# Optimization experiments

Hardware: AMD Instinct MI355X
Metric: run time of the kernel (lower is better)

## Reference

```python
import jax, jax.numpy as jnp
import numpy as np

B, D, H, DM, O = 8192, 512, 1024, 2048, 256


def setup_inputs() -> dict:
    key = jax.random.key(0)
    ks = jax.random.split(key, 24)
    def rn(k, shape, scale=1.0):
        return jax.random.normal(k, shape, dtype=jnp.float32) * scale
    w = 0.02  # weight init scale
    return {
        "x":  rn(ks[0], (B, D)),
        "h0": rn(ks[1], (B, H), 0.1), "h1": rn(ks[2], (B, H), 0.1),
        "c0": rn(ks[3], (B, H), 0.1), "c1": rn(ks[4], (B, H), 0.1),
        # Bernoulli keep masks with model_prob=1.0 -> all ones
        "m0": jnp.ones((B, H), jnp.float32), "m1": jnp.ones((B, H), jnp.float32),
        # layer 0 gate weights: in = D + H = 1536
        "Wf0": rn(ks[5], (D + H, H), w), "bf0": jnp.full((H,), 0.01, jnp.float32),
        "Wi0": rn(ks[6], (D + H, H), w), "bi0": jnp.full((H,), 0.01, jnp.float32),
        "Wc0": rn(ks[7], (D + H, H), w), "bc0": jnp.full((H,), 0.01, jnp.float32),
        "Wo0": rn(ks[8], (D + H, H), w), "bo0": jnp.full((H,), 0.01, jnp.float32),
        # layer 1 gate weights: in = H + H = 2048
        "Wf1": rn(ks[9],  (2 * H, H), w), "bf1": jnp.full((H,), 0.01, jnp.float32),
        "Wi1": rn(ks[10], (2 * H, H), w), "bi1": jnp.full((H,), 0.01, jnp.float32),
        "Wc1": rn(ks[11], (2 * H, H), w), "bc1": jnp.full((H,), 0.01, jnp.float32),
        "Wo1": rn(ks[12], (2 * H, H), w), "bo1": jnp.full((H,), 0.01, jnp.float32),
        # output MLP: H -> DM -> O (identity activation per default nn.Sequential())
        "Wm1": rn(ks[13], (H, DM), w), "bm1": jnp.full((DM,), 0.01, jnp.float32),
        "Wm2": rn(ks[14], (DM, O), w), "bm2": jnp.full((O,), 0.01, jnp.float32),
    }


def _lstm_cell(comb, c, Wf, bf, Wi, bi, Wc, bc, Wo, bo):
    # fuse the 4 gate GEMMs into one matmul, then split
    W = jnp.concatenate([Wf, Wi, Wc, Wo], axis=1)      # [in, 4H]
    b = jnp.concatenate([bf, bi, bc, bo])               # [4H]
    g = comb @ W + b                                    # [B, 4H]
    f, i, ct, o = jnp.split(g, 4, axis=1)
    c_new = jax.nn.sigmoid(f) * c + jax.nn.sigmoid(i) * jnp.tanh(ct)
    h_new = jax.nn.sigmoid(o) * jnp.tanh(c_new)
    return h_new, c_new


def reference(x, h0, h1, c0, c1, m0, m1,
              Wf0, bf0, Wi0, bi0, Wc0, bc0, Wo0, bo0,
              Wf1, bf1, Wi1, bi1, Wc1, bc1, Wo1, bo1,
              Wm1, bm1, Wm2, bm2):
    # layer 0: combined = cat(input, h0 * mask0)
    comb0 = jnp.concatenate([x, h0 * m0], axis=1)       # [B, D+H]
    h0n, c0n = _lstm_cell(comb0, c0, Wf0, bf0, Wi0, bi0, Wc0, bc0, Wo0, bo0)
    # layer 1: combined = cat(h0_new * mask0, h1 * mask1)
    comb1 = jnp.concatenate([h0n * m0, h1 * m1], axis=1)  # [B, 2H]
    h1n, c1n = _lstm_cell(comb1, c1, Wf1, bf1, Wi1, bi1, Wc1, bc1, Wo1, bo1)
    # output MLP (dropout p=0 is identity; activation is identity Sequential)
    out = (h1n @ Wm1 + bm1) @ Wm2 + bm2                 # [B, O]
    return out, h0n, h1n, c0n, c1n
```

## Files before the change

kernel.cpp:

```cpp
#include <hip/hip_runtime.h>
#include <hip/hip_bf16.h>
#include <cstdint>
#include <cstddef>

#define DI __device__ __forceinline__

typedef __attribute__((ext_vector_type(8))) short short8;
typedef __attribute__((ext_vector_type(4))) float f32x4;

static constexpr int Bb = 8192, Dd = 512, Hh = 1024;

DI short f2b(float f) {
  union { __hip_bfloat16 h; short s; } u;
  u.h = __float2bfloat16(f);
  return u.s;
}

DI float sigm(float x) {
  float e = __builtin_amdgcn_exp2f(-1.4426950408889634f * x);
  return __builtin_amdgcn_rcpf(1.0f + e);
}
DI float tanh_(float x) {
  float xc = fminf(fmaxf(x, -20.0f), 20.0f);
  float e = __builtin_amdgcn_exp2f(-2.8853900817779268f * xc);
  return (1.0f - e) * __builtin_amdgcn_rcpf(1.0f + e);
}

DI void gload16(const void* g, void* l) {
  __builtin_amdgcn_global_load_lds(
      (const __attribute__((address_space(1))) uint32_t*)g,
      (__attribute__((address_space(3))) uint32_t*)l, 16, 0, 0);
}


__global__ void conv_acts(const float* __restrict__ x, const float* __restrict__ h0,
                          const float* __restrict__ m0, const float* __restrict__ h1,
                          const float* __restrict__ m1,
                          short* __restrict__ A0, short* __restrict__ A1) {
  const int row = blockIdx.x, t = threadIdx.x;
  float v[8];
  if (t < 192) {
    if (t < 64) {
      const float4* p = (const float4*)(x + (size_t)row * Dd + t * 8);
      float4 a = p[0], b = p[1];
      v[0] = a.x; v[1] = a.y; v[2] = a.z; v[3] = a.w;
      v[4] = b.x; v[5] = b.y; v[6] = b.z; v[7] = b.w;
    } else {
      const int j = t * 8 - 512;
      const float4* ph = (const float4*)(h0 + (size_t)row * Hh + j);
      const float4* pm = (const float4*)(m0 + (size_t)row * Hh + j);
      float4 a = ph[0], b = ph[1], ma = pm[0], mb = pm[1];
      v[0] = a.x * ma.x; v[1] = a.y * ma.y; v[2] = a.z * ma.z; v[3] = a.w * ma.w;
      v[4] = b.x * mb.x; v[5] = b.y * mb.y; v[6] = b.z * mb.z; v[7] = b.w * mb.w;
    }
    short8 o;
    #pragma unroll
    for (int q = 0; q < 8; q++) o[q] = f2b(v[q]);
    *(short8*)(A0 + (size_t)row * 1536 + t * 8) = o;
  } else {
    const int j = (t - 192) * 8;
    const float4* ph = (const float4*)(h1 + (size_t)row * Hh + j);
    const float4* pm = (const float4*)(m1 + (size_t)row * Hh + j);
    float4 a = ph[0], b = ph[1], ma = pm[0], mb = pm[1];
    v[0] = a.x * ma.x; v[1] = a.y * ma.y; v[2] = a.z * ma.z; v[3] = a.w * ma.w;
    v[4] = b.x * mb.x; v[5] = b.y * mb.y; v[6] = b.z * mb.z; v[7] = b.w * mb.w;
    short8 o;
    #pragma unroll
    for (int q = 0; q < 8; q++) o[q] = f2b(v[q]);
    *(short8*)(A1 + (size_t)row * 2048 + 1024 + j) = o;
  }
}

__global__ void transpose_conv4(const float* __restrict__ s0, const float* __restrict__ s1,
                                const float* __restrict__ s2, const float* __restrict__ s3,
                                short* __restrict__ dst, int N, int K) {
  __shared__ float t[64][65];
  const int g = blockIdx.z;
  const float* src = (g == 0) ? s0 : (g == 1) ? s1 : (g == 2) ? s2 : s3;
  const int k0 = blockIdx.x * 64, n0 = blockIdx.y * 64;
  const int tid = threadIdx.x;
  const int r = tid >> 2, c0 = (tid & 3) * 16;
  const float* s = src + (size_t)(k0 + r) * N + n0 + c0;
  #pragma unroll
  for (int q = 0; q < 16; q += 4) {
    float4 v = *(const float4*)(s + q);
    t[r][c0 + q + 0] = v.x; t[r][c0 + q + 1] = v.y;
    t[r][c0 + q + 2] = v.z; t[r][c0 + q + 3] = v.w;
  }
  __syncthreads();
  const int n = n0 + r;
  const int j = (n >> 4) * 64 + g * 16 + (n & 15);
  short8 o0, o1;
  #pragma unroll
  for (int q = 0; q < 8; q++) o0[q] = f2b(t[c0 + q][r]);
  #pragma unroll
  for (int q = 0; q < 8; q++) o1[q] = f2b(t[c0 + 8 + q][r]);
  short* d = dst + (size_t)j * K + k0 + c0;
  *(short8*)d = o0;
  *((short8*)d + 1) = o1;
}

__global__ void transpose_conv(const float* __restrict__ src, short* __restrict__ dst,
                               int N, int K) {
  __shared__ float t[64][65];
  const int k0 = blockIdx.x * 64, n0 = blockIdx.y * 64;
  const int tid = threadIdx.x;
  const int r = tid >> 2, c0 = (tid & 3) * 16;
  const float* s = src + (size_t)(k0 + r) * N + n0 + c0;
  #pragma unroll
  for (int q = 0; q < 16; q += 4) {
    float4 v = *(const float4*)(s + q);
    t[r][c0 + q + 0] = v.x; t[r][c0 + q + 1] = v.y;
    t[r][c0 + q + 2] = v.z; t[r][c0 + q + 3] = v.w;
  }
  __syncthreads();
  const int n = n0 + r;
  short8 o0, o1;
  #pragma unroll
  for (int q = 0; q < 8; q++) o0[q] = f2b(t[c0 + q][r]);
  #pragma unroll
  for (int q = 0; q < 8; q++) o1[q] = f2b(t[c0 + 8 + q][r]);
  short* d = dst + (size_t)n * K + k0 + c0;
  *(short8*)d = o0;
  *((short8*)d + 1) = o1;
}

__global__ void conv_plain(const float* __restrict__ src, short* __restrict__ dst, int n8) {
  const int id = blockIdx.x * blockDim.x + threadIdx.x;
  if (id >= n8) return;
  const float4* p = (const float4*)(src + (size_t)id * 8);
  float4 a = p[0], b = p[1];
  short8 o;
  o[0] = f2b(a.x); o[1] = f2b(a.y); o[2] = f2b(a.z); o[3] = f2b(a.w);
  o[4] = f2b(b.x); o[5] = f2b(b.y); o[6] = f2b(b.z); o[7] = f2b(b.w);
  *(short8*)(dst + (size_t)id * 8) = o;
}

__global__ void bp_init(const float* __restrict__ bm2, float* __restrict__ bp) {
  bp[threadIdx.x] = bm2[threadIdx.x];
}
__global__ void bp_acc(const float* __restrict__ bm1, const float* __restrict__ Wm2,
                       float* __restrict__ bp) {
  const int o = threadIdx.x;
  const int k0 = blockIdx.x * 64;
  float s = 0.f;
  #pragma unroll 4
  for (int k = 0; k < 64; k++) s += bm1[k0 + k] * Wm2[(size_t)(k0 + k) * 256 + o];
  atomicAdd(&bp[o], s);
}

__global__ __launch_bounds__(256) void gemm_bt0(
    const short* __restrict__ A, const short* __restrict__ Bt, int K,
    short* __restrict__ Cb, int ldc) {
  __shared__ __align__(16) short sA[128 * 32];
  __shared__ __align__(16) short sB[128 * 32];
  const int tid = threadIdx.x;
  const int lane = tid & 63;
  const int wave = tid >> 6;
  const int wm = wave >> 1, wn = wave & 1;
  const int bm = blockIdx.x, bn = blockIdx.y;
  const int lr = lane & 15, lq = lane >> 4;

  f32x4 acc[4][4] = {};

  const short* pA = A + ((size_t)(bm * 128 + (tid >> 2))) * K + (tid & 3) * 8;
  const short* pB = Bt + ((size_t)(bn * 128 + (tid >> 2))) * K + (tid & 3) * 8;
  short* lA = sA + tid * 8;
  short* lB = sB + tid * 8;
  const int aoff = (wm * 64 + lr) * 32 + lq * 8;
  const int boff = (wn * 64 + lr) * 32 + lq * 8;

  for (int k0 = 0; k0 < K; k0 += 32) {
    gload16(pA + k0, lA);
    gload16(pA + (size_t)64 * K + k0, lA + 2048);
    gload16(pB + k0, lB);
    gload16(pB + (size_t)64 * K + k0, lB + 2048);
    __syncthreads();
    short8 af[4], bv[4];
    #pragma unroll
    for (int m = 0; m < 4; m++) af[m] = *(const short8*)&sA[aoff + m * 512];
    #pragma unroll
    for (int n = 0; n < 4; n++) bv[n] = *(const short8*)&sB[boff + n * 512];
    #pragma unroll
    for (int m = 0; m < 4; m++)
      #pragma unroll
      for (int n = 0; n < 4; n++)
        acc[m][n] = __builtin_amdgcn_mfma_f32_16x16x32_bf16(af[m], bv[n], acc[m][n], 0, 0, 0);
    __syncthreads();
  }

  const int crow0 = bm * 128 + wm * 64 + lq * 4;
  const int ccol0 = bn * 128 + wn * 64 + lr;
  #pragma unroll
  for (int m = 0; m < 4; m++)
    #pragma unroll
    for (int r = 0; r < 4; r++) {
      const int row = crow0 + m * 16 + r;
      #pragma unroll
      for (int n = 0; n < 4; n++)
        Cb[(size_t)row * ldc + ccol0 + n * 16] = f2b(acc[m][n][r]);
    }
}

__global__ __launch_bounds__(256) void gemm_out(
    const short* __restrict__ A, const short* __restrict__ Bt, int K,
    float* __restrict__ outp, const float* __restrict__ bpv) {
  __shared__ __align__(16) short sA[64 * 32];
  __shared__ __align__(16) short sB[128 * 32];
  const int tid = threadIdx.x;
  const int lane = tid & 63;
  const int wn = tid >> 6;
  const int bm = blockIdx.x, bn = blockIdx.y;
  const int lr = lane & 15, lq = lane >> 4;

  f32x4 acc[4][2] = {};

  const short* pA = A + ((size_t)(bm * 64 + (tid >> 2))) * K + (tid & 3) * 8;
  const short* pB = Bt + ((size_t)(bn * 128 + (tid >> 2))) * K + (tid & 3) * 8;
  short* lA = sA + tid * 8;
  short* lB = sB + tid * 8;
  const int boff = (wn * 32 + lr) * 32 + lq * 8;

  for (int k0 = 0; k0 < K; k0 += 32) {
    gload16(pA + k0, lA);
    gload16(pB + k0, lB);
    gload16(pB + (size_t)64 * K + k0, lB + 2048);
    __syncthreads();
    short8 af[4], bv[2];
    #pragma unroll
    for (int m = 0; m < 4; m++) af[m] = *(const short8*)&sA[(m * 16 + lr) * 32 + lq * 8];
    #pragma unroll
    for (int n = 0; n < 2; n++) bv[n] = *(const short8*)&sB[boff + n * 512];
    #pragma unroll
    for (int m = 0; m < 4; m++)
      #pragma unroll
      for (int n = 0; n < 2; n++)
        acc[m][n] = __builtin_amdgcn_mfma_f32_16x16x32_bf16(af[m], bv[n], acc[m][n], 0, 0, 0);
    __syncthreads();
  }

  const int crow0 = bm * 64 + lq * 4;
  const int ccol0 = bn * 128 + wn * 32 + lr;
  float bvv[2];
  #pragma unroll
  for (int n = 0; n < 2; n++) bvv[n] = bpv[ccol0 + n * 16];
  #pragma unroll
  for (int m = 0; m < 4; m++)
    #pragma unroll
    for (int r = 0; r < 4; r++) {
      const int row = crow0 + m * 16 + r;
      #pragma unroll
      for (int n = 0; n < 2; n++)
        outp[(size_t)row * 256 + ccol0 + n * 16] = acc[m][n][r] + bvv[n];
    }
}


#define STA(buf, h, kt) { const short* s_ = gA + (size_t)(h) * 64 * K + (size_t)(kt) * 64; \
    gload16(s_ + aS0, &sA[buf][h][tid * 8]);                                               \
    gload16(s_ + aS1, &sA[buf][h][4096 + tid * 8]); }
#define STB(buf, h, kt) { const short* s_ = gB + (size_t)(h) * 128 * K + (size_t)(kt) * 64; \
    gload16(s_ + bS0, &sB[buf][h][tid * 8]);                                                \
    gload16(s_ + bS1, &sB[buf][h][4096 + tid * 8]); }

#define LDB(buf) {                                                \
    const short* bb = &sB[buf][bh][brb];                          \
    _Pragma("unroll") for (int n = 0; n < 4; n++) {               \
      bv[n][0] = *(const short8*)(bb + n * 1024 + sw0);           \
      bv[n][1] = *(const short8*)(bb + n * 1024 + sw1); } }

#define LDA_(buf, q, av) {                                        \
    const short* ab = &sA[buf][(q) >> 1][arb + ((q) & 1) * 2048]; \
    av[0][0] = *(const short8*)(ab + sw0);                        \
    av[0][1] = *(const short8*)(ab + sw1);                        \
    av[1][0] = *(const short8*)(ab + 1024 + sw0);                 \
    av[1][1] = *(const short8*)(ab + 1024 + sw1); }

#define MM(q, av) {                                               \
    __builtin_amdgcn_s_setprio(1);                                \
    _Pragma("unroll") for (int m = 0; m < 2; m++)                 \
    _Pragma("unroll") for (int n = 0; n < 4; n++) {               \
      acc[2*(q)+m][n] = __builtin_amdgcn_mfma_f32_16x16x32_bf16(av[m][0], bv[n][0], acc[2*(q)+m][n], 0, 0, 0); \
      acc[2*(q)+m][n] = __builtin_amdgcn_mfma_f32_16x16x32_bf16(av[m][1], bv[n][1], acc[2*(q)+m][n], 0, 0, 0); } \
    __builtin_amdgcn_s_setprio(0); }

#define BARR() __builtin_amdgcn_s_barrier()
#define VM6()  asm volatile("s_waitcnt vmcnt(6)")
#define LG0()  asm volatile("s_waitcnt lgkmcnt(0)")

__global__ __launch_bounds__(512, 2) void gemm8_lstm(
    const short* __restrict__ A, const short* __restrict__ Bt, const int K,
    const float* __restrict__ cprev, float* __restrict__ hout,
    float* __restrict__ cout, short* __restrict__ anext, const int ldan,
    const float* __restrict__ mask,
    const float* __restrict__ bF, const float* __restrict__ bI,
    const float* __restrict__ bC, const float* __restrict__ bO) {
  __shared__ __align__(16) short sA[2][2][8192];
  __shared__ __align__(16) short sB[2][2][8192];
  const int tid = threadIdx.x;
  const int lane = tid & 63, wid = tid >> 6;
  const int wr = wid >> 2, wc = wid & 3;
  const int lr = lane & 15, lq = lane >> 4;
  const int bm = blockIdx.x, bn = blockIdx.y;

  const int NT = K >> 6;
  const int NIT = NT >> 1;

  const int r0 = tid >> 3;
  const int csw = (tid & 7) ^ (r0 & 7);
  const int growA0 = ((r0 >> 5) & 1) * 32 + (r0 & 31);
  const int growA1 = 128 + growA0;
  const size_t aS0 = (size_t)growA0 * K + csw * 8;
  const size_t aS1 = (size_t)growA1 * K + csw * 8;
  const size_t bS0 = (size_t)r0 * K + csw * 8;
  const size_t bS1 = (size_t)(r0 + 64) * K + csw * 8;
  const short* gA = A + (size_t)bm * 256 * K;
  const short* gB = Bt + (size_t)bn * 256 * K;

  const int arb = (wr * 64 + lr) * 64;
  const int brb = ((wc & 1) * 64 + lr) * 64;
  const int bh = wc >> 1;
  const int sw0 = ((lq) ^ (lr & 7)) * 8;
  const int sw1 = ((4 + lq) ^ (lr & 7)) * 8;

  f32x4 acc[8][4] = {};
  short8 bv[4][2];

  STB(0, 0, 0); STB(0, 1, 0); STA(0, 0, 0); STA(0, 1, 0);
  STB(1, 0, 1); STB(1, 1, 1); STA(1, 0, 1);
  VM6(); BARR();

  for (int it = 0; it < NIT; ++it) {
    const int k1 = 2 * it + 1;
    int t2 = 2 * it + 2; if (t2 >= NT) t2 = 0;
    int t3 = 2 * it + 3; if (t3 >= NT) t3 = 1;
    { short8 av0[2][2], av1[2][2];
      LDB(0); LDA_(0, 0, av0); LDA_(0, 1, av1); STA(1, 1, k1);
      BARR(); LG0(); MM(0, av0); MM(1, av1); BARR(); }
    { short8 av0[2][2], av1[2][2];
      LDA_(0, 2, av0); LDA_(0, 3, av1);
      STB(0, 0, t2); STB(0, 1, t2); STA(0, 0, t2);
      VM6(); BARR(); LG0(); MM(2, av0); MM(3, av1); BARR(); }
    { short8 av0[2][2], av1[2][2];
      LDB(1); LDA_(1, 0, av0); LDA_(1, 1, av1); STA(0, 1, t2);
      BARR(); LG0(); MM(0, av0); MM(1, av1); BARR(); }
    { short8 av0[2][2], av1[2][2];
      LDA_(1, 2, av0); LDA_(1, 3, av1);
      STB(1, 0, t3); STB(1, 1, t3); STA(1, 0, t3);
      VM6(); BARR(); LG0(); MM(2, av0); MM(3, av1); BARR(); }
  }

  const int n = (bn * 4 + wc) * 16 + lr;
  const float bf_ = bF[n], bi_ = bI[n], bc_ = bC[n], bo_ = bO[n];
  const int row0 = bm * 256 + wr * 128 + lq * 4;

  float cp[4], mk[4], cpn[4], mkn[4];
  #pragma unroll
  for (int rr = 0; rr < 4; rr++) {
    const size_t idx = (size_t)(row0 + rr) * 1024 + n;
    cp[rr] = cprev[idx];
    mk[rr] = mask ? mask[idx] : 1.0f;
  }
  #pragma unroll
  for (int mf = 0; mf < 8; mf++) {
    if (mf < 7) {
      #pragma unroll
      for (int rr = 0; rr < 4; rr++) {
        const size_t idx2 = (size_t)(row0 + (mf + 1) * 16 + rr) * 1024 + n;
        cpn[rr] = cprev[idx2];
        mkn[rr] = mask ? mask[idx2] : 1.0f;
      }
    }
    #pragma unroll
    for (int rr = 0; rr < 4; rr++) {
      const int row = row0 + mf * 16 + rr;
      const size_t idx = (size_t)row * 1024 + n;
      const float fg = sigm(acc[mf][0][rr] + bf_);
      const float ig = sigm(acc[mf][1][rr] + bi_);
      const float cg = tanh_(acc[mf][2][rr] + bc_);
      const float og = sigm(acc[mf][3][rr] + bo_);
      const float cn = fg * cp[rr] + ig * cg;
      const float hn = og * tanh_(cn);
      cout[idx] = cn;
      hout[idx] = hn;
      anext[(size_t)row * ldan + n] = f2b(hn * mk[rr]);
    }
    #pragma unroll
    for (int rr = 0; rr < 4; rr++) { cp[rr] = cpn[rr]; mk[rr] = mkn[rr]; }
  }
}


extern "C" void kernel_launch(void* const* d_in, const int* in_sizes, int n_in,
                              void* d_out, int out_size, void* d_ws, size_t ws_size,
                              hipStream_t stream) {
  (void)in_sizes; (void)n_in; (void)out_size; (void)ws_size;
  const float* x   = (const float*)d_in[0];
  const float* h0  = (const float*)d_in[1];
  const float* h1  = (const float*)d_in[2];
  const float* c0  = (const float*)d_in[3];
  const float* c1  = (const float*)d_in[4];
  const float* m0  = (const float*)d_in[5];
  const float* m1  = (const float*)d_in[6];
  const float* Wf0 = (const float*)d_in[7];  const float* bf0 = (const float*)d_in[8];
  const float* Wi0 = (const float*)d_in[9];  const float* bi0 = (const float*)d_in[10];
  const float* Wc0 = (const float*)d_in[11]; const float* bc0 = (const float*)d_in[12];
  const float* Wo0 = (const float*)d_in[13]; const float* bo0 = (const float*)d_in[14];
  const float* Wf1 = (const float*)d_in[15]; const float* bf1 = (const float*)d_in[16];
  const float* Wi1 = (const float*)d_in[17]; const float* bi1 = (const float*)d_in[18];
  const float* Wc1 = (const float*)d_in[19]; const float* bc1 = (const float*)d_in[20];
  const float* Wo1 = (const float*)d_in[21]; const float* bo1 = (const float*)d_in[22];
  const float* Wm1 = (const float*)d_in[23]; const float* bm1 = (const float*)d_in[24];
  const float* Wm2 = (const float*)d_in[25]; const float* bm2 = (const float*)d_in[26];

  float* dout  = (float*)d_out;
  float* out_o = dout;
  float* h0n   = dout + 2097152;
  float* h1n   = h0n + 8388608;
  float* c0n   = h1n + 8388608;
  float* c1n   = c0n + 8388608;

  char* ws = (char*)d_ws;
  short* A0   = (short*)(ws);
  short* A1   = (short*)(ws + 25165824);
  short* A2   = (short*)(ws + 58720256);
  short* WT0  = (short*)(ws + 75497472);
  short* WT1  = (short*)(ws + 88080384);
  short* Wm1b = (short*)(ws + 104857600);
  short* Wm2T = (short*)(ws + 109051904);
  short* WpT  = (short*)(ws + 110100480);
  float* bp   = (float*)(ws + 110624768);

  conv_acts<<<dim3(8192), dim3(320), 0, stream>>>(x, h0, m0, h1, m1, A0, A1);
  transpose_conv4<<<dim3(24, 16, 4), dim3(256), 0, stream>>>(Wf0, Wi0, Wc0, Wo0, WT0, 1024, 1536);
  transpose_conv4<<<dim3(32, 16, 4), dim3(256), 0, stream>>>(Wf1, Wi1, Wc1, Wo1, WT1, 1024, 2048);
  conv_plain<<<dim3(1024), dim3(256), 0, stream>>>(Wm1, Wm1b, 262144);
  transpose_conv<<<dim3(32, 4), dim3(256), 0, stream>>>(Wm2, Wm2T, 256, 2048);
  bp_init<<<dim3(1), dim3(256), 0, stream>>>(bm2, bp);
  bp_acc<<<dim3(32), dim3(256), 0, stream>>>(bm1, Wm2, bp);

  gemm_bt0<<<dim3(2, 8), dim3(256), 0, stream>>>(Wm2T, Wm1b, 2048, WpT, 1024);

  gemm8_lstm<<<dim3(32, 16), dim3(512), 0, stream>>>(
      A0, WT0, 1536, c0, h0n, c0n, A1, 2048, m0, bf0, bi0, bc0, bo0);

  gemm8_lstm<<<dim3(32, 16), dim3(512), 0, stream>>>(
      A1, WT1, 2048, c1, h1n, c1n, A2, 1024, nullptr, bf1, bi1, bc1, bo1);

  gemm_out<<<dim3(128, 2), dim3(256), 0, stream>>>(A2, WpT, 1024, out_o, bp);
}
```

Baseline: 406.6 us.

## Merge weight-prep kernels and spread global-to-LDS stores across finer MFMA phases

Six preprocessing launches (two gate-weight transposes, Wm1 conversion, Wm2 transpose, bias init and accumulate) become two kernels: one transposes both layers' gate weights and one handles all MLP prep, including a non-atomic bias reduction. This cuts launch overhead and idle tails between small kernels. The LSTM GEMM main loop now runs eight phases per iteration instead of four, each with one A fragment load and one staged global store, plus a partial lgkmcnt wait. The aim is to interleave memory traffic more evenly with MFMA work, at the price of twice as many barriers per iteration.

```diff
diff --git a/kernel.cpp b/kernel.cpp
--- a/kernel.cpp
+++ b/kernel.cpp
@@ -71,16 +71,30 @@
   }
 }
 
-__global__ void transpose_conv4(const float* __restrict__ s0, const float* __restrict__ s1,
-                                const float* __restrict__ s2, const float* __restrict__ s3,
-                                short* __restrict__ dst, int N, int K) {
+__global__ void transpose_all(
+    const float* __restrict__ w00, const float* __restrict__ w01,
+    const float* __restrict__ w02, const float* __restrict__ w03,
+    const float* __restrict__ w10, const float* __restrict__ w11,
+    const float* __restrict__ w12, const float* __restrict__ w13,
+    short* __restrict__ WT0, short* __restrict__ WT1) {
   __shared__ float t[64][65];
-  const int g = blockIdx.z;
-  const float* src = (g == 0) ? s0 : (g == 1) ? s1 : (g == 2) ? s2 : s3;
-  const int k0 = blockIdx.x * 64, n0 = blockIdx.y * 64;
+  const int z = blockIdx.z;
+  const int layer = z >> 2, g = z & 3;
+  const int K = layer ? 2048 : 1536;
+  const int k0 = blockIdx.x * 64;
+  if (k0 >= K) return;
+  const float* src;
+  switch (z) {
+    case 0: src = w00; break; case 1: src = w01; break;
+    case 2: src = w02; break; case 3: src = w03; break;
+    case 4: src = w10; break; case 5: src = w11; break;
+    case 6: src = w12; break; default: src = w13; break;
+  }
+  short* dst = layer ? WT1 : WT0;
+  const int n0 = blockIdx.y * 64;
   const int tid = threadIdx.x;
   const int r = tid >> 2, c0 = (tid & 3) * 16;
-  const float* s = src + (size_t)(k0 + r) * N + n0 + c0;
+  const float* s = src + (size_t)(k0 + r) * 1024 + n0 + c0;
   #pragma unroll
   for (int q = 0; q < 16; q += 4) {
     float4 v = *(const float4*)(s + q);
@@ -100,53 +114,59 @@
   *((short8*)d + 1) = o1;
 }
 
-__global__ void transpose_conv(const float* __restrict__ src, short* __restrict__ dst,
-                               int N, int K) {
+__global__ void mlp_prep(const float* __restrict__ Wm1, short* __restrict__ Wm1b,
+                         const float* __restrict__ Wm2, short* __restrict__ Wm2T,
+                         const float* __restrict__ bm1, const float* __restrict__ bm2,
+                         float* __restrict__ bp) {
   __shared__ float t[64][65];
-  const int k0 = blockIdx.x * 64, n0 = blockIdx.y * 64;
-  const int tid = threadIdx.x;
-  const int r = tid >> 2, c0 = (tid & 3) * 16;
-  const float* s = src + (size_t)(k0 + r) * N + n0 + c0;
-  #pragma unroll
-  for (int q = 0; q < 16; q += 4) {
-    float4 v = *(const float4*)(s + q);
-    t[r][c0 + q + 0] = v.x; t[r][c0 + q + 1] = v.y;
-    t[r][c0 + q + 2] = v.z; t[r][c0 + q + 3] = v.w;
-  }
-  __syncthreads();
-  const int n = n0 + r;
-  short8 o0, o1;
-  #pragma unroll
-  for (int q = 0; q < 8; q++) o0[q] = f2b(t[c0 + q][r]);
-  #pragma unroll
-  for (int q = 0; q < 8; q++) o1[q] = f2b(t[c0 + 8 + q][r]);
-  short* d = dst + (size_t)n * K + k0 + c0;
-  *(short8*)d = o0;
-  *((short8*)d + 1) = o1;
-}
-
-__global__ void conv_plain(const float* __restrict__ src, short* __restrict__ dst, int n8) {
-  const int id = blockIdx.x * blockDim.x + threadIdx.x;
-  if (id >= n8) return;
-  const float4* p = (const float4*)(src + (size_t)id * 8);
-  float4 a = p[0], b = p[1];
-  short8 o;
-  o[0] = f2b(a.x); o[1] = f2b(a.y); o[2] = f2b(a.z); o[3] = f2b(a.w);
-  o[4] = f2b(b.x); o[5] = f2b(b.y); o[6] = f2b(b.z); o[7] = f2b(b.w);
-  *(short8*)(dst + (size_t)id * 8) = o;
-}
-
-__global__ void bp_init(const float* __restrict__ bm2, float* __restrict__ bp) {
-  bp[threadIdx.x] = bm2[threadIdx.x];
-}
-__global__ void bp_acc(const float* __restrict__ bm1, const float* __restrict__ Wm2,
-                       float* __restrict__ bp) {
-  const int o = threadIdx.x;
-  const int k0 = blockIdx.x * 64;
-  float s = 0.f;
-  #pragma unroll 4
-  for (int k = 0; k < 64; k++) s += bm1[k0 + k] * Wm2[(size_t)(k0 + k) * 256 + o];
-  atomicAdd(&bp[o], s);
+  const int b = blockIdx.x, tid = threadIdx.x;
+  if (b < 1024) {
+    const int id = b * 256 + tid;
+    const float4* p = (const float4*)(Wm1 + (size_t)id * 8);
+    float4 a = p[0], bb = p[1];
+    short8 o;
+    o[0] = f2b(a.x); o[1] = f2b(a.y); o[2] = f2b(a.z); o[3] = f2b(a.w);
+    o[4] = f2b(bb.x); o[5] = f2b(bb.y); o[6] = f2b(bb.z); o[7] = f2b(bb.w);
+    *(short8*)(Wm1b + (size_t)id * 8) = o;
+  } else if (b < 1152) {
+    const int b2 = b - 1024;
+    const int k0 = (b2 & 31) * 64, n0 = (b2 >> 5) * 64;
+    const int r = tid >> 2, c0 = (tid & 3) * 16;
+    const float* s = Wm2 + (size_t)(k0 + r) * 256 + n0 + c0;
+    #pragma unroll
+    for (int q = 0; q < 16; q += 4) {
+      float4 v = *(const float4*)(s + q);
+      t[r][c0 + q + 0] = v.x; t[r][c0 + q + 1] = v.y;
+      t[r][c0 + q + 2] = v.z; t[r][c0 + q + 3] = v.w;
+    }
+    __syncthreads();
+    const int n = n0 + r;
+    short8 o0, o1;
+    #pragma unroll
+    for (int q = 0; q < 8; q++) o0[q] = f2b(t[c0 + q][r]);
+    #pragma unroll
+    for (int q = 0; q < 8; q++) o1[q] = f2b(t[c0 + 8 + q][r]);
+    short* d = Wm2T + (size_t)n * 2048 + k0 + c0;
+    *(short8*)d = o0;
+    *((short8*)d + 1) = o1;
+  } else {
+    __shared__ float red[16][17];
+    const int o0 = (b - 1152) * 16;
+    const int oo = tid & 15, kk = tid >> 4;
+    float s = 0.f;
+    const int kbase = kk * 128;
+    #pragma unroll 4
+    for (int k = 0; k < 128; k++)
+      s += bm1[kbase + k] * Wm2[(size_t)(kbase + k) * 256 + o0 + oo];
+    red[kk][oo] = s;
+    __syncthreads();
+    if (tid < 16) {
+      float acc = bm2[o0 + tid];
+      #pragma unroll
+      for (int j = 0; j < 16; j++) acc += red[j][tid];
+      bp[o0 + tid] = acc;
+    }
+  }
 }
 
 __global__ __launch_bounds__(256) void gemm_bt0(
@@ -286,7 +306,11 @@
 
 #define BARR() __builtin_amdgcn_s_barrier()
 #define VM6()  asm volatile("s_waitcnt vmcnt(6)")
+#define LG8()  asm volatile("s_waitcnt lgkmcnt(8)")
 #define LG0()  asm volatile("s_waitcnt lgkmcnt(0)")
+
+#define PH(buf, q, STG, vm) { short8 av[2][2]; LDA_(buf, q, av); STG; \
+    if (vm) VM6(); BARR(); LG0(); MM(q, av); BARR(); }
 
 __global__ __launch_bounds__(512, 2) void gemm8_lstm(
     const short* __restrict__ A, const short* __restrict__ Bt, const int K,
@@ -334,20 +358,16 @@
     const int k1 = 2 * it + 1;
     int t2 = 2 * it + 2; if (t2 >= NT) t2 = 0;
     int t3 = 2 * it + 3; if (t3 >= NT) t3 = 1;
-    { short8 av0[2][2], av1[2][2];
-      LDB(0); LDA_(0, 0, av0); LDA_(0, 1, av1); STA(1, 1, k1);
-      BARR(); LG0(); MM(0, av0); MM(1, av1); BARR(); }
-    { short8 av0[2][2], av1[2][2];
-      LDA_(0, 2, av0); LDA_(0, 3, av1);
-      STB(0, 0, t2); STB(0, 1, t2); STA(0, 0, t2);
-      VM6(); BARR(); LG0(); MM(2, av0); MM(3, av1); BARR(); }
-    { short8 av0[2][2], av1[2][2];
-      LDB(1); LDA_(1, 0, av0); LDA_(1, 1, av1); STA(0, 1, t2);
-      BARR(); LG0(); MM(0, av0); MM(1, av1); BARR(); }
-    { short8 av0[2][2], av1[2][2];
-      LDA_(1, 2, av0); LDA_(1, 3, av1);
-      STB(1, 0, t3); STB(1, 1, t3); STA(1, 0, t3);
-      VM6(); BARR(); LG0(); MM(2, av0); MM(3, av1); BARR(); }
+    { short8 av[2][2]; LDB(0); LDA_(0, 0, av); STA(1, 1, k1);
+      LG8(); BARR(); LG0(); MM(0, av); BARR(); }
+    PH(0, 1, STB(0, 0, t2), 0);
+    PH(0, 2, STB(0, 1, t2), 0);
+    PH(0, 3, STA(0, 0, t2), 1);
+    { short8 av[2][2]; LDB(1); LDA_(1, 0, av); STA(0, 1, t2);
+      LG8(); BARR(); LG0(); MM(0, av); BARR(); }
+    PH(1, 1, STB(1, 0, t3), 0);
+    PH(1, 2, STB(1, 1, t3), 0);
+    PH(1, 3, STA(1, 0, t3), 1);
   }
 
   const int n = (bn * 4 + wc) * 16 + lr;
@@ -432,12 +452,9 @@
   float* bp   = (float*)(ws + 110624768);
 
   conv_acts<<<dim3(8192), dim3(320), 0, stream>>>(x, h0, m0, h1, m1, A0, A1);
-  transpose_conv4<<<dim3(24, 16, 4), dim3(256), 0, stream>>>(Wf0, Wi0, Wc0, Wo0, WT0, 1024, 1536);
-  transpose_conv4<<<dim3(32, 16, 4), dim3(256), 0, stream>>>(Wf1, Wi1, Wc1, Wo1, WT1, 1024, 2048);
-  conv_plain<<<dim3(1024), dim3(256), 0, stream>>>(Wm1, Wm1b, 262144);
-  transpose_conv<<<dim3(32, 4), dim3(256), 0, stream>>>(Wm2, Wm2T, 256, 2048);
-  bp_init<<<dim3(1), dim3(256), 0, stream>>>(bm2, bp);
-  bp_acc<<<dim3(32), dim3(256), 0, stream>>>(bm1, Wm2, bp);
+  transpose_all<<<dim3(32, 16, 8), dim3(256), 0, stream>>>(
+      Wf0, Wi0, Wc0, Wo0, Wf1, Wi1, Wc1, Wo1, WT0, WT1);
+  mlp_prep<<<dim3(1168), dim3(256), 0, stream>>>(Wm1, Wm1b, Wm2, Wm2T, bm1, bm2, bp);
 
   gemm_bt0<<<dim3(2, 8), dim3(256), 0, stream>>>(Wm2T, Wm1b, 2048, WpT, 1024);
 
```

After: 391.7 us, median of 2. 1.04x faster.
